# Kernel optimization log

Hardware: AMD Instinct MI355X
Metric: run time of the kernel (lower is better)

Reference implementation:

```python
import jax, jax.numpy as jnp
import numpy as np

B, S, U, H = 4, 2048, 1024, 16
DH = U // H  # head dim = 64
EPS = 1e-8


def setup_inputs() -> dict:
    key = jax.random.key(0)
    ks = jax.random.split(key, 7)
    scale = 1.0 / np.sqrt(U)
    return {
        "queries": jax.random.normal(ks[0], (B, S, U), jnp.float32),
        "keys": jax.random.normal(ks[1], (B, S, U), jnp.float32),
        "values": jax.random.normal(ks[2], (B, S, U), jnp.float32),
        "Wq": jax.random.normal(ks[3], (U, U), jnp.float32) * scale,
        "bq": jnp.zeros((U,), jnp.float32),
        "Wk": jax.random.normal(ks[4], (U, U), jnp.float32) * scale,
        "bk": jnp.zeros((U,), jnp.float32),
        "Wv": jax.random.normal(ks[5], (U, U), jnp.float32) * scale,
        "bv": jnp.zeros((U,), jnp.float32),
        "Wr": jax.random.normal(ks[6], (U, U), jnp.float32) * scale,
        "br": jnp.zeros((U,), jnp.float32),
        "gamma": jnp.ones((U,), jnp.float32),
        "beta": jnp.zeros((U,), jnp.float32),
    }


def reference(queries, keys, values, Wq, bq, Wk, bk, Wv, bv, Wr, br, gamma, beta):
    relu = jax.nn.relu
    Q = relu(queries @ Wq + bq)           # [B,S,U]
    K = relu(keys @ Wk + bk)
    V = relu(values @ Wv + bv)
    V_res = relu(values @ Wr + br)        # residual branch

    # split heads: tf.split(axis=2) + concat(axis=0) == per-head attention
    Qh = Q.reshape(B, S, H, DH)
    Kh = K.reshape(B, S, H, DH)
    Vh = V.reshape(B, S, H, DH)

    scores = jnp.einsum("bshd,bthd->bhst", Qh, Kh) / jnp.sqrt(jnp.float32(DH))
    w = jax.nn.softmax(scores, axis=-1)   # dropout keep_prob=1 -> identity
    out = jnp.einsum("bhst,bthd->bshd", w, Vh).reshape(B, S, U)

    out = relu(out + V_res)

    # manual LayerNorm (eps inside sqrt)
    mean = jnp.mean(out, axis=-1, keepdims=True)
    var = jnp.mean(jnp.square(out - mean), axis=-1, keepdims=True)
    normalized = (out - mean) / jnp.sqrt(var + EPS)
    return gamma * normalized + beta
```

## Files before the change

### kernel.cpp

```cpp
#include <hip/hip_runtime.h>

constexpr int B = 4, S = 2048, U = 1024, H = 16, DH = 64;
constexpr int MTOT = B * S;
constexpr int NT = S / 64;

using bf16   = __bf16;
using f32x4  = __attribute__((ext_vector_type(4))) float;
using f32x16 = __attribute__((ext_vector_type(16))) float;
using bf16x8 = __attribute__((ext_vector_type(8))) bf16;
using bf16x4 = __attribute__((ext_vector_type(4))) bf16;
using u32x4  = __attribute__((ext_vector_type(4))) unsigned int;

__device__ __forceinline__ void gload16(const bf16* g, bf16* l) {
  __builtin_amdgcn_global_load_lds(
      (const __attribute__((address_space(1))) unsigned int*)g,
      (__attribute__((address_space(3))) unsigned int*)l, 16, 0, 0);
}

__device__ __forceinline__ float fexp2(float x) {
#if __has_builtin(__builtin_amdgcn_exp2f)
  return __builtin_amdgcn_exp2f(x);
#else
  return __expf(x * 0.6931471805599453f);
#endif
}

__device__ __forceinline__ f32x16 mfma32(bf16x8 a, bf16x8 b, f32x16 c) {
  return __builtin_amdgcn_mfma_f32_32x32x16_bf16(a, b, c, 0, 0, 0);
}

__device__ __forceinline__ unsigned packbf(float a, float b) {
  union { bf16 h; unsigned short s; } ua, ub;
  ua.h = (bf16)a; ub.h = (bf16)b;
  return ((unsigned)ub.s << 16) | (unsigned)ua.s;
}

__device__ __forceinline__ size_t kpack_off(int M_, int col) {
  const int b = M_ >> 11, s = M_ & 2047;
  const int h = col >> 6, d = col & 63;
  const int bh = b * 16 + h;
  const int t = s >> 6, r64 = s & 63;
  const int tt = r64 >> 5, l31 = r64 & 31;
  const int ks = d >> 4, hi = (d >> 3) & 1, j = d & 7;
  const int ln = l31 + (hi << 5);
  return ((size_t)(bh * 32 + t) << 12) + (tt << 11) + (ks << 9) + (ln << 3) + j;
}

__device__ __forceinline__ size_t vpack_off(int M_, int col) {
  const int b = M_ >> 11, s = M_ & 2047;
  const int h = col >> 6, d = col & 63;
  const int bh = b * 16 + h;
  const int j = s & 7, hi = (s >> 3) & 1, ks = (s >> 4) & 3, t = s >> 6;
  const int dt = d >> 5, l31 = d & 31;
  const int ln = l31 + (hi << 5);
  return ((size_t)(bh * 32 + t) << 12) + (dt << 11) + (ks << 9) + (ln << 3) + j;
}

__global__ __launch_bounds__(256) void prep_kernel(
    const float* __restrict__ xq, const float* __restrict__ xk, const float* __restrict__ xv,
    bf16* __restrict__ oq, bf16* __restrict__ ok, bf16* __restrict__ ov,
    const float* __restrict__ w0, const float* __restrict__ w1,
    const float* __restrict__ w2, const float* __restrict__ w3,
    bf16* __restrict__ t0, bf16* __restrict__ t1,
    bf16* __restrict__ t2, bf16* __restrict__ t3) {
  __shared__ float tile[32][33];
  const int bid = blockIdx.x;
  const int t = threadIdx.x;
  if (bid < 12288) {
    const int z = bid >> 12, idx = bid & 4095;
    const float* x = z == 0 ? xq : z == 1 ? xk : xv;
    bf16* o       = z == 0 ? oq : z == 1 ? ok : ov;
    const size_t i = ((size_t)idx * 256 + t) * 8;
    const float4 v0 = *reinterpret_cast<const float4*>(x + i);
    const float4 v1 = *reinterpret_cast<const float4*>(x + i + 4);
    bf16x8 r;
    r[0] = (bf16)v0.x; r[1] = (bf16)v0.y; r[2] = (bf16)v0.z; r[3] = (bf16)v0.w;
    r[4] = (bf16)v1.x; r[5] = (bf16)v1.y; r[6] = (bf16)v1.z; r[7] = (bf16)v1.w;
    *reinterpret_cast<bf16x8*>(o + i) = r;
  } else {
    const int wb = bid - 12288;
    const int z = wb >> 10, ti = wb & 1023;
    const float* W = z == 0 ? w0 : z == 1 ? w1 : z == 2 ? w2 : w3;
    bf16* Wt       = z == 0 ? t0 : z == 1 ? t1 : z == 2 ? t2 : t3;
    const int k0 = (ti & 31) * 32, n0 = (ti >> 5) * 32;
    const int tx = t & 31, ty = t >> 5;
    for (int i = ty; i < 32; i += 8) tile[i][tx] = W[(size_t)(k0 + i) * U + n0 + tx];
    __syncthreads();
    for (int i = ty; i < 32; i += 8) Wt[(size_t)(n0 + i) * U + k0 + tx] = (bf16)tile[tx][i];
  }
}

__global__ __launch_bounds__(256) void gemm4_kernel(
    const bf16* __restrict__ Qc, const bf16* __restrict__ Kc, const bf16* __restrict__ Vc,
    const bf16* __restrict__ wqt, const bf16* __restrict__ wkt,
    const bf16* __restrict__ wvt, const bf16* __restrict__ wrt,
    const float* __restrict__ bq, const float* __restrict__ bk,
    const float* __restrict__ bv, const float* __restrict__ br,
    bf16* __restrict__ oq, bf16* __restrict__ okp,
    bf16* __restrict__ ovp, bf16* __restrict__ orr) {
  const int bid = blockIdx.x;
  const int wg = (bid & 7) * 256 + (bid >> 3);
  const int z = wg >> 9, rem = wg & 511;
  const int bm = (rem >> 3) * 128, bn = (rem & 7) * 128;

  const bf16* A     = z == 0 ? Qc : z == 1 ? Kc : Vc;
  const bf16* Wt    = z == 0 ? wqt : z == 1 ? wkt : z == 2 ? wvt : wrt;
  const float* bias = z == 0 ? bq : z == 1 ? bk : z == 2 ? bv : br;

  const int t = threadIdx.x, lane = t & 63, wid = t >> 6;
  const int wr = wid >> 1, wc = wid & 1;
  const int lm = lane & 15, hi = lane >> 4;

  __shared__ __align__(16) bf16 As[128][64];
  __shared__ __align__(16) bf16 Bs[128][64];

  f32x4 acc[4][4];
#pragma unroll
  for (int i = 0; i < 4; ++i)
#pragma unroll
    for (int j = 0; j < 4; ++j) acc[i][j] = f32x4{0.f, 0.f, 0.f, 0.f};

  const int lr = lane >> 3;
  const int scol = ((lane & 7) ^ lr) * 8;
  const bf16* ga = A  + (size_t)(bm + wid * 32 + lr) * U + scol;
  const bf16* gb = Wt + (size_t)(bn + wid * 32 + lr) * U + scol;

  for (int k0 = 0; k0 < U; k0 += 64) {
    __syncthreads();
#pragma unroll
    for (int p = 0; p < 4; ++p) {
      gload16(ga + (size_t)(p * 8) * U + k0, &As[wid * 32 + p * 8][0]);
      gload16(gb + (size_t)(p * 8) * U + k0, &Bs[wid * 32 + p * 8][0]);
    }
    __syncthreads();

#pragma unroll
    for (int ksub = 0; ksub < 2; ++ksub) {
      const int so = (((ksub * 4 + hi) ^ (lm & 7)) * 16);
      bf16x8 a[4], bb[4];
#pragma unroll
      for (int mi = 0; mi < 4; ++mi)
        a[mi] = *reinterpret_cast<const bf16x8*>(
            reinterpret_cast<const char*>(&As[wr * 64 + mi * 16 + lm][0]) + so);
#pragma unroll
      for (int ni = 0; ni < 4; ++ni)
        bb[ni] = *reinterpret_cast<const bf16x8*>(
            reinterpret_cast<const char*>(&Bs[wc * 64 + ni * 16 + lm][0]) + so);
#pragma unroll
      for (int mi = 0; mi < 4; ++mi)
#pragma unroll
        for (int ni = 0; ni < 4; ++ni)
          acc[mi][ni] = __builtin_amdgcn_mfma_f32_16x16x32_bf16(a[mi], bb[ni], acc[mi][ni], 0, 0, 0);
    }
  }

  const int mb = bm + wr * 64 + hi * 4;
  const int nb = bn + wc * 64 + lm;
  if (z == 1) {
#pragma unroll
    for (int ni = 0; ni < 4; ++ni) {
      const float bv_ = bias[nb + ni * 16];
#pragma unroll
      for (int mi = 0; mi < 4; ++mi)
#pragma unroll
        for (int r = 0; r < 4; ++r) {
          const float vv = fmaxf(acc[mi][ni][r] + bv_, 0.f);
          okp[kpack_off(mb + mi * 16 + r, nb + ni * 16)] = (bf16)vv;
        }
    }
  } else if (z == 2) {
#pragma unroll
    for (int ni = 0; ni < 4; ++ni) {
      const float bv_ = bias[nb + ni * 16];
#pragma unroll
      for (int mi = 0; mi < 4; ++mi)
#pragma unroll
        for (int r = 0; r < 4; ++r) {
          const float vv = fmaxf(acc[mi][ni][r] + bv_, 0.f);
          ovp[vpack_off(mb + mi * 16 + r, nb + ni * 16)] = (bf16)vv;
        }
    }
  } else {
    bf16* out = z == 0 ? oq : orr;
#pragma unroll
    for (int ni = 0; ni < 4; ++ni) {
      const float bv_ = bias[nb + ni * 16];
#pragma unroll
      for (int mi = 0; mi < 4; ++mi)
#pragma unroll
        for (int r = 0; r < 4; ++r) {
          const float vv = fmaxf(acc[mi][ni][r] + bv_, 0.f);
          out[(size_t)(mb + mi * 16 + r) * U + nb + ni * 16] = (bf16)vv;
        }
    }
  }
}

__global__ __launch_bounds__(256, 2) void attn_kernel(
    const bf16* __restrict__ Q, const bf16* __restrict__ Kp,
    const bf16* __restrict__ Vp, bf16* __restrict__ att) {
  const int bid = blockIdx.x;
  const int swz = (bid & 7) * 128 + (bid >> 3);
  const int bh = swz >> 4, qx = swz & 15;
  const int b = bh >> 4, h = bh & 15;
  const int tid = threadIdx.x;
  const int w = tid >> 6, lane = tid & 63;
  const int l31 = lane & 31, hi8 = lane >> 5;
  const int q0 = qx * 128 + w * 32;

  __shared__ __align__(16) bf16 kv[2][8192];

  const float qscale = 0.18033688011111606f;

  const bf16* qbase = Q + ((size_t)b * S + q0 + l31) * U + h * DH + hi8 * 8;
  bf16x8 qf[4];
#pragma unroll
  for (int ks = 0; ks < 4; ++ks) {
    bf16x8 v = *reinterpret_cast<const bf16x8*>(qbase + ks * 16);
#pragma unroll
    for (int j = 0; j < 8; ++j) v[j] = (bf16)((float)v[j] * qscale);
    qf[ks] = v;
  }

  bf16x8 onesf;
#pragma unroll
  for (int j = 0; j < 8; ++j) onesf[j] = (bf16)1.f;

  f32x16 o0 = (f32x16)0.f, o1 = (f32x16)0.f, osum = (f32x16)0.f;

  const bf16* kpb = Kp + (size_t)bh * 32 * 4096;
  const bf16* vpb = Vp + (size_t)bh * 32 * 4096;

  auto stagekv = [&](int buf, int t) {
    const size_t toff = (size_t)t * 4096;
    gload16(kpb + toff + tid * 8,        &kv[buf][tid * 8]);
    gload16(kpb + toff + 2048 + tid * 8, &kv[buf][2048 + tid * 8]);
    gload16(vpb + toff + tid * 8,        &kv[buf][4096 + tid * 8]);
    gload16(vpb + toff + 2048 + tid * 8, &kv[buf][6144 + tid * 8]);
  };

  stagekv(0, 0);
  asm volatile("s_waitcnt vmcnt(0)" ::: "memory");
  __builtin_amdgcn_s_barrier();
  __builtin_amdgcn_sched_barrier(0);

  for (int t = 0; t < NT; ++t) {
    const int cur = t & 1;
    if (t + 1 < NT) stagekv(cur ^ 1, t + 1);

    bf16x8 kf[2][4];
#pragma unroll
    for (int tt = 0; tt < 2; ++tt)
#pragma unroll
      for (int ks = 0; ks < 4; ++ks)
        kf[tt][ks] = *reinterpret_cast<const bf16x8*>(&kv[cur][(tt * 4 + ks) * 512 + lane * 8]);

    f32x16 s0 = (f32x16)0.f, s1 = (f32x16)0.f;
    __builtin_amdgcn_s_setprio(1);
#pragma unroll
    for (int ks = 0; ks < 4; ++ks) {
      s0 = mfma32(kf[0][ks], qf[ks], s0);
      s1 = mfma32(kf[1][ks], qf[ks], s1);
    }
    __builtin_amdgcn_s_setprio(0);

    bf16x8 vf[2][4];
#pragma unroll
    for (int dt = 0; dt < 2; ++dt)
#pragma unroll
      for (int ks = 0; ks < 4; ++ks)
        vf[dt][ks] = *reinterpret_cast<const bf16x8*>(&kv[cur][4096 + (dt * 4 + ks) * 512 + lane * 8]);

    unsigned wpk[16];
#pragma unroll
    for (int i = 0; i < 8; ++i) {
      wpk[i]     = packbf(fexp2(s0[2 * i]), fexp2(s0[2 * i + 1]));
      wpk[8 + i] = packbf(fexp2(s1[2 * i]), fexp2(s1[2 * i + 1]));
    }

    u32x4 fw[4];
#pragma unroll
    for (int fi = 0; fi < 4; ++fi) {
      unsigned a0 = wpk[fi * 4 + 0], b0 = wpk[fi * 4 + 2];
      unsigned a1 = wpk[fi * 4 + 1], b1 = wpk[fi * 4 + 3];
      asm("v_permlane32_swap_b32 %0, %1" : "+v"(a0), "+v"(b0));
      asm("v_permlane32_swap_b32 %0, %1" : "+v"(a1), "+v"(b1));
      fw[fi] = u32x4{a0, a1, b0, b1};
    }

    __builtin_amdgcn_s_setprio(1);
#pragma unroll
    for (int ks = 0; ks < 4; ++ks) {
      const bf16x8 pf = __builtin_bit_cast(bf16x8, fw[ks]);
      o0   = mfma32(pf, vf[0][ks], o0);
      o1   = mfma32(pf, vf[1][ks], o1);
      osum = mfma32(pf, onesf, osum);
    }
    __builtin_amdgcn_s_setprio(0);

    if (t + 1 < NT) {
      asm volatile("s_waitcnt vmcnt(0)" ::: "memory");
      __builtin_amdgcn_s_barrier();
      __builtin_amdgcn_sched_barrier(0);
    }
  }

  bf16* obase = att + ((size_t)b * S + q0) * U + h * DH + l31;
#pragma unroll
  for (int r = 0; r < 16; ++r) {
    const int row = (r & 3) + 8 * (r >> 2) + 4 * hi8;
    const float lr = 1.f / osum[r];
    obase[(size_t)row * U]      = (bf16)(o0[r] * lr);
    obase[(size_t)row * U + 32] = (bf16)(o1[r] * lr);
  }
}

__global__ __launch_bounds__(256) void ln_kernel(
    const bf16* __restrict__ att, const bf16* __restrict__ vres,
    const float* __restrict__ gamma, const float* __restrict__ beta,
    float* __restrict__ out) {
  const int w = threadIdx.x >> 6, lane = threadIdx.x & 63;
  const int row = blockIdx.x * 4 + w;
  const int c0 = lane * 16;
  const bf16* ar = att  + (size_t)row * U + c0;
  const bf16* vr = vres + (size_t)row * U + c0;

  const bf16x8 a0 = *reinterpret_cast<const bf16x8*>(ar);
  const bf16x8 a1 = *reinterpret_cast<const bf16x8*>(ar + 8);
  const bf16x8 v0 = *reinterpret_cast<const bf16x8*>(vr);
  const bf16x8 v1 = *reinterpret_cast<const bf16x8*>(vr + 8);

  float x[16];
  float sum = 0.f, sq = 0.f;
#pragma unroll
  for (int i = 0; i < 8; ++i) {
    x[i]     = fmaxf((float)a0[i] + (float)v0[i], 0.f);
    x[8 + i] = fmaxf((float)a1[i] + (float)v1[i], 0.f);
  }
#pragma unroll
  for (int i = 0; i < 16; ++i) { sum += x[i]; sq += x[i] * x[i]; }
#pragma unroll
  for (int mm = 1; mm < 64; mm <<= 1) {
    sum += __shfl_xor(sum, mm);
    sq  += __shfl_xor(sq, mm);
  }
  const float mean = sum * (1.f / U);
  float var = sq * (1.f / U) - mean * mean;
  var = fmaxf(var, 0.f);
  const float inv = rsqrtf(var + 1e-8f);

  float* orow = out + (size_t)row * U + c0;
#pragma unroll
  for (int j = 0; j < 4; ++j) {
    const float4 g = *reinterpret_cast<const float4*>(gamma + c0 + j * 4);
    const float4 bt = *reinterpret_cast<const float4*>(beta + c0 + j * 4);
    float4 o;
    o.x = g.x * ((x[j * 4 + 0] - mean) * inv) + bt.x;
    o.y = g.y * ((x[j * 4 + 1] - mean) * inv) + bt.y;
    o.z = g.z * ((x[j * 4 + 2] - mean) * inv) + bt.z;
    o.w = g.w * ((x[j * 4 + 3] - mean) * inv) + bt.w;
    *reinterpret_cast<float4*>(orow + j * 4) = o;
  }
}

extern "C" void kernel_launch(void* const* d_in, const int* in_sizes, int n_in,
                              void* d_out, int out_size, void* d_ws, size_t ws_size,
                              hipStream_t stream) {
  const float* queries = (const float*)d_in[0];
  const float* keys    = (const float*)d_in[1];
  const float* values  = (const float*)d_in[2];
  const float* Wq = (const float*)d_in[3];
  const float* bq = (const float*)d_in[4];
  const float* Wk = (const float*)d_in[5];
  const float* bk = (const float*)d_in[6];
  const float* Wv = (const float*)d_in[7];
  const float* bv = (const float*)d_in[8];
  const float* Wr = (const float*)d_in[9];
  const float* br = (const float*)d_in[10];
  const float* gamma = (const float*)d_in[11];
  const float* beta  = (const float*)d_in[12];
  float* out = (float*)d_out;

  char* ws = (char*)d_ws;
  const size_t MB = 1024 * 1024;
  bf16* wqt  = (bf16*)(ws + 0 * MB);
  bf16* wkt  = (bf16*)(ws + 2 * MB);
  bf16* wvt  = (bf16*)(ws + 4 * MB);
  bf16* wrt  = (bf16*)(ws + 6 * MB);
  bf16* Qcvt = (bf16*)(ws + 8 * MB);
  bf16* Kcvt = (bf16*)(ws + 24 * MB);
  bf16* Vcvt = (bf16*)(ws + 40 * MB);
  bf16* Qb   = (bf16*)(ws + 56 * MB);
  bf16* Kp   = (bf16*)(ws + 72 * MB);
  bf16* Vp   = (bf16*)(ws + 88 * MB);
  bf16* attb = Qcvt;
  bf16* Rb   = Kcvt;

  prep_kernel<<<dim3(16384), 256, 0, stream>>>(
      queries, keys, values, Qcvt, Kcvt, Vcvt,
      Wq, Wk, Wv, Wr, wqt, wkt, wvt, wrt);
  gemm4_kernel<<<dim3(2048), 256, 0, stream>>>(
      Qcvt, Kcvt, Vcvt, wqt, wkt, wvt, wrt, bq, bk, bv, br, Qb, Kp, Vp, Rb);
  attn_kernel<<<dim3(1024), 256, 0, stream>>>(Qb, Kp, Vp, attb);
  ln_kernel<<<dim3(MTOT / 4), 256, 0, stream>>>(attb, Rb, gamma, beta, out);
}
```

Before: 210.2 us.

## Enlarge GEMM tiles to 256x256 with double-buffered LDS prefetch interleaved with MFMA

The projection GEMM moves from 128x128 tiles with 256 threads to 256x256 tiles with 512 threads (8 waves, each computing 128x64). Shared memory is double-buffered (128KB), and the next k-slice is fetched by direct global-to-LDS loads spread across the MFMA groups, with setprio raising MFMA priority. The aim is more data reuse per loaded byte, fewer barriers per k-step, and hiding global latency behind compute. The cost is much higher LDS and register use, which limits occupancy, and a smaller grid of 512 blocks that may not balance evenly across CUs.

New measurement: 201.5 us. 4.1% less time.

```diff
diff --git a/kernel.cpp b/kernel.cpp
--- a/kernel.cpp
+++ b/kernel.cpp
@@ -90,7 +90,7 @@
   }
 }
 
-__global__ __launch_bounds__(256) void gemm4_kernel(
+__global__ __launch_bounds__(512, 2) void gemm4_kernel(
     const bf16* __restrict__ Qc, const bf16* __restrict__ Kc, const bf16* __restrict__ Vc,
     const bf16* __restrict__ wqt, const bf16* __restrict__ wkt,
     const bf16* __restrict__ wvt, const bf16* __restrict__ wrt,
@@ -99,69 +99,142 @@
     bf16* __restrict__ oq, bf16* __restrict__ okp,
     bf16* __restrict__ ovp, bf16* __restrict__ orr) {
   const int bid = blockIdx.x;
-  const int wg = (bid & 7) * 256 + (bid >> 3);
-  const int z = wg >> 9, rem = wg & 511;
-  const int bm = (rem >> 3) * 128, bn = (rem & 7) * 128;
+  const int wg = (bid & 7) * 64 + (bid >> 3);
+  const int z = wg >> 7, rem = wg & 127;
+  const int bm = (rem >> 2) * 256, bn = (rem & 3) * 256;
 
   const bf16* A     = z == 0 ? Qc : z == 1 ? Kc : Vc;
   const bf16* Wt    = z == 0 ? wqt : z == 1 ? wkt : z == 2 ? wvt : wrt;
   const float* bias = z == 0 ? bq : z == 1 ? bk : z == 2 ? bv : br;
 
-  const int t = threadIdx.x, lane = t & 63, wid = t >> 6;
-  const int wr = wid >> 1, wc = wid & 1;
+  const int tid = threadIdx.x, lane = tid & 63, w = tid >> 6;
+  const int wr = w >> 2, wcn = w & 3;
   const int lm = lane & 15, hi = lane >> 4;
 
-  __shared__ __align__(16) bf16 As[128][64];
-  __shared__ __align__(16) bf16 Bs[128][64];
-
-  f32x4 acc[4][4];
-#pragma unroll
-  for (int i = 0; i < 4; ++i)
+  __shared__ __align__(16) bf16 smem[65536];
+
+  f32x4 acc[8][4];
+#pragma unroll
+  for (int i = 0; i < 8; ++i)
 #pragma unroll
     for (int j = 0; j < 4; ++j) acc[i][j] = f32x4{0.f, 0.f, 0.f, 0.f};
 
-  const int lr = lane >> 3;
-  const int scol = ((lane & 7) ^ lr) * 8;
-  const bf16* ga = A  + (size_t)(bm + wid * 32 + lr) * U + scol;
-  const bf16* gb = Wt + (size_t)(bn + wid * 32 + lr) * U + scol;
-
-  for (int k0 = 0; k0 < U; k0 += 64) {
-    __syncthreads();
-#pragma unroll
-    for (int p = 0; p < 4; ++p) {
-      gload16(ga + (size_t)(p * 8) * U + k0, &As[wid * 32 + p * 8][0]);
-      gload16(gb + (size_t)(p * 8) * U + k0, &Bs[wid * 32 + p * 8][0]);
-    }
-    __syncthreads();
-
-#pragma unroll
-    for (int ksub = 0; ksub < 2; ++ksub) {
-      const int so = (((ksub * 4 + hi) ^ (lm & 7)) * 16);
-      bf16x8 a[4], bb[4];
-#pragma unroll
-      for (int mi = 0; mi < 4; ++mi)
-        a[mi] = *reinterpret_cast<const bf16x8*>(
-            reinterpret_cast<const char*>(&As[wr * 64 + mi * 16 + lm][0]) + so);
-#pragma unroll
-      for (int ni = 0; ni < 4; ++ni)
-        bb[ni] = *reinterpret_cast<const bf16x8*>(
-            reinterpret_cast<const char*>(&Bs[wc * 64 + ni * 16 + lm][0]) + so);
-#pragma unroll
-      for (int mi = 0; mi < 4; ++mi)
-#pragma unroll
-        for (int ni = 0; ni < 4; ++ni)
-          acc[mi][ni] = __builtin_amdgcn_mfma_f32_16x16x32_bf16(a[mi], bb[ni], acc[mi][ni], 0, 0, 0);
-    }
-  }
-
-  const int mb = bm + wr * 64 + hi * 4;
-  const int nb = bn + wc * 64 + lm;
+  const int srow = tid >> 3, sslot = tid & 7;
+  const int scol = (sslot ^ (srow & 7)) * 8;
+  const bf16* gA = A  + (size_t)(bm + srow) * U + scol;
+  const bf16* gB = Wt + (size_t)(bn + srow) * U + scol;
+
+  auto stageA = [&](int buf, int half, int k0) {
+    bf16* l = smem + buf * 32768 + (half * 128 + srow) * 64 + sslot * 8;
+    gload16(gA + (size_t)(half * 128) * U + k0, l);
+    gload16(gA + (size_t)(half * 128 + 64) * U + k0, l + 64 * 64);
+  };
+  auto stageB = [&](int buf, int half, int k0) {
+    bf16* l = smem + buf * 32768 + 16384 + (half * 128 + srow) * 64 + sslot * 8;
+    gload16(gB + (size_t)(half * 128) * U + k0, l);
+    gload16(gB + (size_t)(half * 128 + 64) * U + k0, l + 64 * 64);
+  };
+
+  auto loadA = [&](int buf, int mi, int ks) {
+    const int row = wr * 128 + mi * 16 + lm;
+    const int slot = (ks * 4 + hi) ^ (lm & 7);
+    return *reinterpret_cast<const bf16x8*>(smem + buf * 32768 + row * 64 + slot * 8);
+  };
+  auto loadB = [&](int buf, int ni, int ks) {
+    const int row = wcn * 64 + ni * 16 + lm;
+    const int slot = (ks * 4 + hi) ^ (lm & 7);
+    return *reinterpret_cast<const bf16x8*>(smem + buf * 32768 + 16384 + row * 64 + slot * 8);
+  };
+
+  stageA(0, 0, 0); stageA(0, 1, 0); stageB(0, 0, 0); stageB(0, 1, 0);
+  asm volatile("s_waitcnt vmcnt(0)" ::: "memory");
+  __builtin_amdgcn_s_barrier();
+  __builtin_amdgcn_sched_barrier(0);
+
+  for (int t = 0; t < 16; ++t) {
+    const int buf = t & 1, nbf = buf ^ 1;
+    const int k1 = (t + 1) * 64;
+    const bool pre = (t + 1) < 16;
+
+    bf16x8 bfr[4][2];
+
+    if (pre) stageA(nbf, 0, k1);
+#pragma unroll
+    for (int ni = 0; ni < 4; ++ni) {
+      bfr[ni][0] = loadB(buf, ni, 0);
+      bfr[ni][1] = loadB(buf, ni, 1);
+    }
+    {
+      bf16x8 a00 = loadA(buf, 0, 0), a01 = loadA(buf, 0, 1);
+      bf16x8 a10 = loadA(buf, 1, 0), a11 = loadA(buf, 1, 1);
+      __builtin_amdgcn_s_setprio(1);
+#pragma unroll
+      for (int ni = 0; ni < 4; ++ni) {
+        acc[0][ni] = __builtin_amdgcn_mfma_f32_16x16x32_bf16(a00, bfr[ni][0], acc[0][ni], 0, 0, 0);
+        acc[0][ni] = __builtin_amdgcn_mfma_f32_16x16x32_bf16(a01, bfr[ni][1], acc[0][ni], 0, 0, 0);
+        acc[1][ni] = __builtin_amdgcn_mfma_f32_16x16x32_bf16(a10, bfr[ni][0], acc[1][ni], 0, 0, 0);
+        acc[1][ni] = __builtin_amdgcn_mfma_f32_16x16x32_bf16(a11, bfr[ni][1], acc[1][ni], 0, 0, 0);
+      }
+      __builtin_amdgcn_s_setprio(0);
+    }
+    if (pre) stageA(nbf, 1, k1);
+    {
+      bf16x8 a00 = loadA(buf, 2, 0), a01 = loadA(buf, 2, 1);
+      bf16x8 a10 = loadA(buf, 3, 0), a11 = loadA(buf, 3, 1);
+      __builtin_amdgcn_s_setprio(1);
+#pragma unroll
+      for (int ni = 0; ni < 4; ++ni) {
+        acc[2][ni] = __builtin_amdgcn_mfma_f32_16x16x32_bf16(a00, bfr[ni][0], acc[2][ni], 0, 0, 0);
+        acc[2][ni] = __builtin_amdgcn_mfma_f32_16x16x32_bf16(a01, bfr[ni][1], acc[2][ni], 0, 0, 0);
+        acc[3][ni] = __builtin_amdgcn_mfma_f32_16x16x32_bf16(a10, bfr[ni][0], acc[3][ni], 0, 0, 0);
+        acc[3][ni] = __builtin_amdgcn_mfma_f32_16x16x32_bf16(a11, bfr[ni][1], acc[3][ni], 0, 0, 0);
+      }
+      __builtin_amdgcn_s_setprio(0);
+    }
+    if (pre) stageB(nbf, 0, k1);
+    {
+      bf16x8 a00 = loadA(buf, 4, 0), a01 = loadA(buf, 4, 1);
+      bf16x8 a10 = loadA(buf, 5, 0), a11 = loadA(buf, 5, 1);
+      __builtin_amdgcn_s_setprio(1);
+#pragma unroll
+      for (int ni = 0; ni < 4; ++ni) {
+        acc[4][ni] = __builtin_amdgcn_mfma_f32_16x16x32_bf16(a00, bfr[ni][0], acc[4][ni], 0, 0, 0);
+        acc[4][ni] = __builtin_amdgcn_mfma_f32_16x16x32_bf16(a01, bfr[ni][1], acc[4][ni], 0, 0, 0);
+        acc[5][ni] = __builtin_amdgcn_mfma_f32_16x16x32_bf16(a10, bfr[ni][0], acc[5][ni], 0, 0, 0);
+        acc[5][ni] = __builtin_amdgcn_mfma_f32_16x16x32_bf16(a11, bfr[ni][1], acc[5][ni], 0, 0, 0);
+      }
+      __builtin_amdgcn_s_setprio(0);
+    }
+    if (pre) stageB(nbf, 1, k1);
+    {
+      bf16x8 a00 = loadA(buf, 6, 0), a01 = loadA(buf, 6, 1);
+      bf16x8 a10 = loadA(buf, 7, 0), a11 = loadA(buf, 7, 1);
+      __builtin_amdgcn_s_setprio(1);
+#pragma unroll
+      for (int ni = 0; ni < 4; ++ni) {
+        acc[6][ni] = __builtin_amdgcn_mfma_f32_16x16x32_bf16(a00, bfr[ni][0], acc[6][ni], 0, 0, 0);
+        acc[6][ni] = __builtin_amdgcn_mfma_f32_16x16x32_bf16(a01, bfr[ni][1], acc[6][ni], 0, 0, 0);
+        acc[7][ni] = __builtin_amdgcn_mfma_f32_16x16x32_bf16(a10, bfr[ni][0], acc[7][ni], 0, 0, 0);
+        acc[7][ni] = __builtin_amdgcn_mfma_f32_16x16x32_bf16(a11, bfr[ni][1], acc[7][ni], 0, 0, 0);
+      }
+      __builtin_amdgcn_s_setprio(0);
+    }
+
+    if (pre) {
+      asm volatile("s_waitcnt vmcnt(0)" ::: "memory");
+      __builtin_amdgcn_s_barrier();
+      __builtin_amdgcn_sched_barrier(0);
+    }
+  }
+
+  const int mb = bm + wr * 128 + hi * 4;
+  const int nb = bn + wcn * 64 + lm;
   if (z == 1) {
 #pragma unroll
     for (int ni = 0; ni < 4; ++ni) {
       const float bv_ = bias[nb + ni * 16];
 #pragma unroll
-      for (int mi = 0; mi < 4; ++mi)
+      for (int mi = 0; mi < 8; ++mi)
 #pragma unroll
         for (int r = 0; r < 4; ++r) {
           const float vv = fmaxf(acc[mi][ni][r] + bv_, 0.f);
@@ -173,7 +246,7 @@
     for (int ni = 0; ni < 4; ++ni) {
       const float bv_ = bias[nb + ni * 16];
 #pragma unroll
-      for (int mi = 0; mi < 4; ++mi)
+      for (int mi = 0; mi < 8; ++mi)
 #pragma unroll
         for (int r = 0; r < 4; ++r) {
           const float vv = fmaxf(acc[mi][ni][r] + bv_, 0.f);
@@ -186,7 +259,7 @@
     for (int ni = 0; ni < 4; ++ni) {
       const float bv_ = bias[nb + ni * 16];
 #pragma unroll
-      for (int mi = 0; mi < 4; ++mi)
+      for (int mi = 0; mi < 8; ++mi)
 #pragma unroll
         for (int r = 0; r < 4; ++r) {
           const float vv = fmaxf(acc[mi][ni][r] + bv_, 0.f);
@@ -399,7 +472,7 @@
   prep_kernel<<<dim3(16384), 256, 0, stream>>>(
       queries, keys, values, Qcvt, Kcvt, Vcvt,
       Wq, Wk, Wv, Wr, wqt, wkt, wvt, wrt);
-  gemm4_kernel<<<dim3(2048), 256, 0, stream>>>(
+  gemm4_kernel<<<dim3(512), 512, 0, stream>>>(
       Qcvt, Kcvt, Vcvt, wqt, wkt, wvt, wrt, bq, bk, bv, br, Qb, Kp, Vp, Rb);
   attn_kernel<<<dim3(1024), 256, 0, stream>>>(Qb, Kp, Vp, attb);
   ln_kernel<<<dim3(MTOT / 4), 256, 0, stream>>>(attb, Rb, gamma, beta, out);
```
